# Kernel optimization log

Hardware: AMD Instinct MI355X
Metric: run time of the kernel (lower is better)

## Reference

```python
import jax, jax.numpy as jnp
import numpy as np

B, N, F, E = 4, 256, 128, 128
HID = 128      # link ConvLSTM hidden channels
L_PROP = 2     # propagate_layers
SUB, AFF = 10, 12


def setup_inputs() -> dict:
    key = jax.random.key(0)
    ks = jax.random.split(key, 16)
    s = 0.02
    inp = dict(
        edge_features=jax.random.normal(ks[0], (B, E, N, N), jnp.float32),
        node_features=jax.random.normal(ks[1], (B, F, N), jnp.float32),
        adj_mat=jax.random.uniform(ks[2], (B, N, N), dtype=jnp.float32),
        node_labels=jnp.zeros((B, N, AFF), jnp.float32),
        args=0,
    )
    # GraphConvLSTM link function: two 1x1-conv LSTM cells + 1x1 output conv
    inp['W_lstm0'] = s * jax.random.normal(ks[3], (4 * HID, E + HID), jnp.float32)
    inp['b_lstm0'] = jnp.zeros((4 * HID,), jnp.float32)
    inp['W_lstm1'] = s * jax.random.normal(ks[4], (4 * HID, HID + HID), jnp.float32)
    inp['b_lstm1'] = jnp.zeros((4 * HID,), jnp.float32)
    inp['W_link_out'] = s * jax.random.normal(ks[5], (1, HID), jnp.float32)
    inp['b_link_out'] = jnp.zeros((1,), jnp.float32)
    # linear_concat message: Linear(2F+E -> E)
    inp['W_msg'] = s * jax.random.normal(ks[6], (E, 2 * F + E), jnp.float32)
    inp['b_msg'] = jnp.zeros((E,), jnp.float32)
    # two GRU update functions (node 0 vs other nodes), input E, hidden F
    inp['Wih0'] = s * jax.random.normal(ks[7], (3 * F, E), jnp.float32)
    inp['Whh0'] = s * jax.random.normal(ks[8], (3 * F, F), jnp.float32)
    inp['bih0'] = jnp.zeros((3 * F,), jnp.float32)
    inp['bhh0'] = jnp.zeros((3 * F,), jnp.float32)
    inp['Wih1'] = s * jax.random.normal(ks[9], (3 * F, E), jnp.float32)
    inp['Whh1'] = s * jax.random.normal(ks[10], (3 * F, F), jnp.float32)
    inp['bih1'] = jnp.zeros((3 * F,), jnp.float32)
    inp['bhh1'] = jnp.zeros((3 * F,), jnp.float32)
    # fc_soft_max readouts
    inp['Wr0'] = s * jax.random.normal(ks[11], (SUB, F), jnp.float32)
    inp['br0'] = jnp.zeros((SUB,), jnp.float32)
    inp['Wr1'] = s * jax.random.normal(ks[12], (AFF, F), jnp.float32)
    inp['br1'] = jnp.zeros((AFF,), jnp.float32)
    return inp


def _link_fun(he, Ws, bs, Wo, bo):
    # he: [B, C, N, N] edge states -> predicted soft adjacency [B, N, N]
    x = he
    for W, b in zip(Ws, bs):
        hid = W.shape[0] // 4
        h0 = jnp.zeros(x.shape[:1] + (hid,) + x.shape[2:], x.dtype)
        xc = jnp.concatenate([x, h0], axis=1)
        g = jnp.einsum('oc,bcvw->bovw', W, xc) + b[None, :, None, None]
        i_g, f_g, g_g, o_g = jnp.split(g, 4, axis=1)
        c = jax.nn.sigmoid(i_g) * jnp.tanh(g_g)  # forget*c0 vanishes (c0=0)
        x = jax.nn.sigmoid(o_g) * jnp.tanh(c)
    a = jnp.einsum('oc,bcvw->bovw', Wo, x) + bo[None, :, None, None]
    return jax.nn.sigmoid(a)[:, 0]  # [B, N, N]


def _messages(node_features, edge_features, A, W_msg, b_msg):
    # X[b,:,w,i] = concat(h_i, h_w, e[i,w]); m[b,o,w,i] = (W_msg X + b) * A[b,i,w]
    hv = jnp.broadcast_to(node_features[:, :, None, :], (B, F, N, N))
    hw = jnp.broadcast_to(node_features[:, :, :, None], (B, F, N, N))
    ev = jnp.swapaxes(edge_features, 2, 3)
    X = jnp.concatenate([hv, hw, ev], axis=1)  # [B, 2F+E, N, N]
    m = jnp.einsum('of,bfwi->bowi', W_msg, X) + b_msg[None, :, None, None]
    return m * jnp.swapaxes(A, 1, 2)[:, None, :, :]


def _gru(x, h, Wih, Whh, bih, bhh):
    gi = x @ Wih.T + bih
    gh = h @ Whh.T + bhh
    ir, iz, inn = jnp.split(gi, 3, axis=-1)
    hr, hz, hn = jnp.split(gh, 3, axis=-1)
    r = jax.nn.sigmoid(ir + hr)
    z = jax.nn.sigmoid(iz + hz)
    n = jnp.tanh(inn + r * hn)
    return (1.0 - z) * n + z * h


def reference(edge_features, node_features, adj_mat, node_labels, args,
              W_lstm0, b_lstm0, W_lstm1, b_lstm1, W_link_out, b_link_out,
              W_msg, b_msg, Wih0, Whh0, bih0, bhh0, Wih1, Whh1, bih1, bhh1,
              Wr0, br0, Wr1, br1):
    he = edge_features  # hidden_edge_states[0]
    A = None
    m_sum = None
    for _ in range(L_PROP):
        A = _link_fun(he, [W_lstm0, W_lstm1], [b_lstm0, b_lstm1], W_link_out, b_link_out)
        m = _messages(node_features, edge_features, A, W_msg, b_msg)
        he = m                     # hidden_edge_states[r+1][:,:,:,i] = m_v
        m_sum = m.sum(axis=2)      # [B, E, N]: sum over source nodes w
    # GRU update (hidden node states are never rewritten in the source, so
    # only the last round's update feeds the readout)
    h = jnp.swapaxes(node_features, 1, 2)  # [B, N, F]
    x = jnp.swapaxes(m_sum, 1, 2)          # [B, N, E]
    h_new0 = _gru(x[:, :1], h[:, :1], Wih0, Whh0, bih0, bhh0)  # node 0
    h_new1 = _gru(x[:, 1:], h[:, 1:], Wih1, Whh1, bih1, bhh1)  # other nodes
    out0 = jax.nn.log_softmax(h_new0[:, 0] @ Wr0.T + br0, axis=-1)  # [B, SUB]
    out1 = jax.nn.log_softmax(h_new1 @ Wr1.T + br1, axis=-1)        # [B, N-1, AFF]
    pred = jnp.zeros(node_labels.shape, node_labels.dtype)
    pred = pred.at[:, 0, :SUB].set(out0)
    pred = pred.at[:, 1:, :].set(out1)
    return A, pred
```

## Files before the change

### kernel.cpp

```cpp
#include <hip/hip_runtime.h>

#define CH 128
#define PIXTOT (4*256*256)
#define L2E 1.4426950408889634f

typedef unsigned short u16;
typedef short short8 __attribute__((ext_vector_type(8)));
typedef float f32x4 __attribute__((ext_vector_type(4)));

__device__ __forceinline__ float bf2f(u16 u){ return __uint_as_float(((unsigned)u)<<16); }
__device__ __forceinline__ u16 f2bf(float f){
  return (u16)((__float_as_uint(f) + 0x8000u) >> 16);
}
__device__ __forceinline__ unsigned pk2(float a, float b){
  return (unsigned)f2bf(a) | ((unsigned)f2bf(b) << 16);
}
__device__ __forceinline__ float fexp2(float x){ return __builtin_amdgcn_exp2f(x); }
__device__ __forceinline__ float frcp(float x){ return __builtin_amdgcn_rcpf(x); }
__device__ __forceinline__ float sigm(float x){ return frcp(1.f + fexp2(-L2E*x)); }
__device__ __forceinline__ float tanh_f(float x){ return 1.f - 2.f*frcp(fexp2(2.f*L2E*x)+1.f); }
__device__ __forceinline__ float pade_tanh(float c){
  float c2 = c*c, c4 = c2*c2;
  float p  = __builtin_fmaf(c2, 105.f, 945.f) + c4;
  float q  = __builtin_fmaf(c4, 15.f, __builtin_fmaf(c2, 420.f, 945.f));
  return c * p * frcp(q);
}

__global__ __launch_bounds__(256) void wcvt_kernel(
    const float* __restrict__ W0, const float* __restrict__ bl0,
    const float* __restrict__ W1, const float* __restrict__ bl1,
    const float* __restrict__ Wm,
    const float* __restrict__ Wih1, const float* __restrict__ Whh1,
    u16* __restrict__ W0c, u16* __restrict__ W1c,
    float* __restrict__ b0c, float* __restrict__ b1c,
    u16* __restrict__ Wmc, float* __restrict__ W3T,
    u16* __restrict__ Wuv, u16* __restrict__ Wg1)
{
  int idx = blockIdx.x*256 + threadIdx.x;
  int col = idx & 127;
  if (idx < 49152){
    int row = idx >> 7;
    int slot = row >> 7;
    int src = (row < 128) ? row : row + 128;
    float s = (slot == 1) ? (2.f*L2E) : (-L2E);
    W0c[idx] = f2bf(W0[(size_t)src*256 + col] * s);
    W1c[idx] = f2bf(W1[(size_t)src*256 + col] * s);
  }
  if (idx < 16384){
    int o = idx >> 7, k = col;
    float w = Wm[(size_t)o*384 + 256 + k];
    Wmc[idx] = f2bf(w);
    W3T[(size_t)k*128 + o] = w;
  }
  if (idx < 32768){
    int row = idx >> 7;
    Wuv[idx] = (row < 128) ? f2bf(Wm[(size_t)row*384 + col])
                           : f2bf(Wm[(size_t)(row-128)*384 + 128 + col]);
  }
  {
    int row = idx >> 7;
    Wg1[idx] = (row < 384) ? f2bf(Wih1[(size_t)row*128 + col])
                           : f2bf(Whh1[(size_t)(row-384)*128 + col]);
  }
  if (idx < 384){
    int row = idx;
    int src = (row < 128) ? row : row + 128;
    float s = ((row>>7) == 1) ? (2.f*L2E) : (-L2E);
    b0c[idx] = bl0[src] * s;
    b1c[idx] = bl1[src] * s;
  }
}

__device__ __forceinline__ void stage_cmaj(
    const float* __restrict__ base, u16 (*xs)[136], int t)
{
  const int cg = t >> 4, pg = t & 15;
  const int c0 = cg*8, p0 = pg*4;
  float v[8][4];
  #pragma unroll
  for (int cc=0; cc<8; cc++){
    const f32x4 f = *(const f32x4*)(base + (size_t)(c0+cc)*256 + p0);
    v[cc][0]=f[0]; v[cc][1]=f[1]; v[cc][2]=f[2]; v[cc][3]=f[3];
  }
  #pragma unroll
  for (int pp=0; pp<4; pp++){
    unsigned d[4];
    #pragma unroll
    for (int q=0; q<4; q++) d[q] = pk2(v[2*q][pp], v[2*q+1][pp]);
    *(uint4*)&xs[p0+pp][c0] = *(const uint4*)d;
  }
}

__global__ __launch_bounds__(256) void uvmfma_kernel(
    const float* __restrict__ nf, const u16* __restrict__ Wuv,
    const float* __restrict__ bmsg, float* __restrict__ U, float* __restrict__ V)
{
  const int b = blockIdx.x >> 2, i0 = (blockIdx.x & 3) * 64;
  __shared__ u16 xs[64][136];
  const int t = threadIdx.x;
  stage_cmaj(nf + (size_t)b*CH*256 + i0, xs, t);
  __syncthreads();
  const int wv = t >> 6, lane = t & 63, lm = lane & 15, quad = lane >> 4;
  f32x4 acc[4][4];
  #pragma unroll
  for (int rs=0; rs<4; rs++)
    #pragma unroll
    for (int nt=0; nt<4; nt++){ f32x4 z={0.f,0.f,0.f,0.f}; acc[rs][nt]=z; }
  #pragma unroll
  for (int k0=0; k0<128; k0+=32){
    short8 bfr[4];
    #pragma unroll
    for (int nt=0; nt<4; nt++)
      bfr[nt] = *(const short8*)&xs[nt*16+lm][k0 + quad*8];
    #pragma unroll
    for (int rs=0; rs<4; rs++){
      const short8 afr = *(const short8*)(Wuv + ((size_t)(wv*64 + rs*16 + lm))*128 + k0 + quad*8);
      #pragma unroll
      for (int nt=0; nt<4; nt++)
        acc[rs][nt] = __builtin_amdgcn_mfma_f32_16x16x32_bf16(afr, bfr[nt], acc[rs][nt], 0,0,0);
    }
  }
  #pragma unroll
  for (int rs=0; rs<4; rs++){
    const int row0 = wv*64 + rs*16 + quad*4;
    #pragma unroll
    for (int nt=0; nt<4; nt++){
      const int i = i0 + nt*16 + lm;
      f32x4 o = acc[rs][nt];
      if (row0 < 128){
        const f32x4 bm = *(const f32x4*)(bmsg + row0);
        o[0]+=bm[0]; o[1]+=bm[1]; o[2]+=bm[2]; o[3]+=bm[3];
        *(f32x4*)(U + ((size_t)(b*256 + i))*CH + row0) = o;
      } else {
        *(f32x4*)(V + ((size_t)(b*256 + i))*CH + row0 - 128) = o;
      }
    }
  }
}

template<bool LAST>
__device__ __forceinline__ void lstm_layer(
    const u16 (*xin)[136], u16 (*xout)[136],
    const u16* __restrict__ W, const float* __restrict__ Bc,
    int oc0, int lm, int quad, const float woc[2][4], float* partial)
{
  float tp[2][4][4];
  #pragma unroll
  for (int g=0; g<3; g++){
    f32x4 acc[2][4];
    #pragma unroll
    for (int rs=0; rs<2; rs++)
      #pragma unroll
      for (int nt=0; nt<4; nt++){ f32x4 z={0.f,0.f,0.f,0.f}; acc[rs][nt]=z; }
    #pragma unroll
    for (int k0=0; k0<128; k0+=32){
      short8 bfr[4];
      #pragma unroll
      for (int nt=0; nt<4; nt++)
        bfr[nt] = *(const short8*)&xin[nt*16+lm][k0 + quad*8];
      #pragma unroll
      for (int rs=0; rs<2; rs++){
        const short8 afr = *(const short8*)(W + ((size_t)(g*128 + oc0 + rs*16 + lm))*128 + k0 + quad*8);
        #pragma unroll
        for (int nt=0; nt<4; nt++)
          acc[rs][nt] = __builtin_amdgcn_mfma_f32_16x16x32_bf16(afr, bfr[nt], acc[rs][nt], 0,0,0);
      }
    }
    #pragma unroll
    for (int rs=0; rs<2; rs++){
      float bi[4];
      #pragma unroll
      for (int r=0; r<4; r++) bi[r] = Bc[g*128 + oc0 + rs*16 + quad*4 + r];
      #pragma unroll
      for (int nt=0; nt<4; nt++){
        if (g == 0){
          #pragma unroll
          for (int r=0; r<4; r++)
            tp[rs][nt][r] = frcp(1.f + fexp2(acc[rs][nt][r] + bi[r]));
        } else if (g == 1){
          #pragma unroll
          for (int r=0; r<4; r++){
            float e = fexp2(fminf(acc[rs][nt][r] + bi[r], 80.f));
            float c = tp[rs][nt][r] * (e - 1.f) * frcp(e + 1.f);
            tp[rs][nt][r] = pade_tanh(c);
          }
        } else {
          float xo[4];
          #pragma unroll
          for (int r=0; r<4; r++)
            xo[r] = tp[rs][nt][r] * frcp(1.f + fexp2(acc[rs][nt][r] + bi[r]));
          if (LAST){
            #pragma unroll
            for (int r=0; r<4; r++)
              partial[nt] = __builtin_fmaf(xo[r], woc[rs][r], partial[nt]);
          } else {
            ushort4 w4;
            #pragma unroll
            for (int r=0; r<4; r++) ((u16*)&w4)[r] = f2bf(xo[r]);
            *(ushort4*)&xout[nt*16+lm][oc0 + rs*16 + quad*4] = w4;
          }
        }
      }
    }
  }
}

template<int MODE>
__global__ __launch_bounds__(256, 3) void link_kernel(
    const float* __restrict__ edge, const float* __restrict__ A1,
    const float* __restrict__ U, const float* __restrict__ V,
    const u16* __restrict__ Wmc,
    const u16* __restrict__ W0c, const float* __restrict__ B0c,
    const u16* __restrict__ W1c, const float* __restrict__ B1c,
    const float* __restrict__ Wo, const float* __restrict__ Bo,
    float* __restrict__ Aout, float* __restrict__ outA, float* __restrict__ A2nat)
{
  __shared__ u16 xs[64][136];
  __shared__ u16 ys[64][136];
  __shared__ float red[64][17];
  const int t = threadIdx.x;
  const int Q0 = blockIdx.x * 64;
  const int b = Q0 >> 16, q1 = (Q0 >> 8) & 255, w0 = Q0 & 255;
  stage_cmaj(edge + ((size_t)b*CH*256 + q1)*256 + w0, xs, t);
  const int wv = t >> 6, lane = t & 63, lm = lane & 15, quad = lane >> 4;
  const int oc0 = wv*32;
  float woc[2][4];
  #pragma unroll
  for (int rs=0; rs<2; rs++){
    const f32x4 wv4 = *(const f32x4*)(Wo + oc0 + rs*16 + quad*4);
    #pragma unroll
    for (int r=0; r<4; r++) woc[rs][r] = wv4[r];
  }
  __syncthreads();
  if (MODE){
    f32x4 acc[2][4];
    #pragma unroll
    for (int rs=0; rs<2; rs++)
      #pragma unroll
      for (int nt=0; nt<4; nt++){ f32x4 z={0.f,0.f,0.f,0.f}; acc[rs][nt]=z; }
    #pragma unroll
    for (int k0=0; k0<128; k0+=32){
      short8 bfr[4];
      #pragma unroll
      for (int nt=0; nt<4; nt++)
        bfr[nt] = *(const short8*)&xs[nt*16+lm][k0 + quad*8];
      #pragma unroll
      for (int rs=0; rs<2; rs++){
        const short8 afr = *(const short8*)(Wmc + ((size_t)(oc0 + rs*16 + lm))*128 + k0 + quad*8);
        #pragma unroll
        for (int nt=0; nt<4; nt++)
          acc[rs][nt] = __builtin_amdgcn_mfma_f32_16x16x32_bf16(afr, bfr[nt], acc[rs][nt], 0,0,0);
      }
    }
    #pragma unroll
    for (int rs=0; rs<2; rs++){
      const int o0 = oc0 + rs*16 + quad*4;
      const f32x4 ug = *(const f32x4*)(U + ((size_t)(b*256 + q1))*CH + o0);
      #pragma unroll
      for (int nt=0; nt<4; nt++){
        const int px = nt*16 + lm;
        const float a1 = A1[Q0 + px];
        const f32x4 vg = *(const f32x4*)(V + ((size_t)(b*256 + w0 + px))*CH + o0);
        ushort4 w4;
        #pragma unroll
        for (int r=0; r<4; r++)
          ((u16*)&w4)[r] = f2bf((acc[rs][nt][r] + ug[r] + vg[r]) * a1);
        *(ushort4*)&ys[px][o0] = w4;
      }
    }
    __syncthreads();
  }
  const u16 (*in0)[136] = MODE ? (const u16(*)[136])ys : (const u16(*)[136])xs;
  u16 (*buf)[136] = MODE ? xs : ys;
  float partial[4] = {0.f, 0.f, 0.f, 0.f};
  lstm_layer<false>(in0, buf, W0c, B0c, oc0, lm, quad, woc, partial);
  __syncthreads();
  lstm_layer<true>((const u16(*)[136])buf, (u16(*)[136])nullptr, W1c, B1c, oc0, lm, quad, woc, partial);
  #pragma unroll
  for (int nt=0; nt<4; nt++) red[nt*16+lm][wv*4+quad] = partial[nt];
  __syncthreads();
  if (t < 64){
    float s = Bo[0];
    #pragma unroll
    for (int k=0; k<16; k++) s += red[t][k];
    const float sg = sigm(s);
    Aout[Q0 + t] = sg;
    if (MODE){
      const size_t p = (size_t)b*65536 + (size_t)(w0 + t)*256 + q1;
      outA[p]  = sg;
      A2nat[p] = sg;
    }
  }
}

__global__ __launch_bounds__(256) void se_kernel(
    const float* __restrict__ edge, const float* __restrict__ A2nat,
    float* __restrict__ s_e, float* __restrict__ sA)
{
  const int b = blockIdx.x >> 8, i = blockIdx.x & 255;
  __shared__ float al[256];
  __shared__ float sb[128][9];
  __shared__ float rr[64];
  const int t = threadIdx.x;
  al[t] = A2nat[((size_t)(b*256 + i))*256 + t];
  __syncthreads();
  const int seg = t & 7, cb = t >> 3;
  #pragma unroll
  for (int cc=0; cc<4; cc++){
    const int c = cc*32 + cb;
    const float* src = edge + (((size_t)(b*CH + c))*256 + i)*256;
    float s = 0.f;
    #pragma unroll
    for (int j=0; j<8; j++){
      const int idx = j*32 + seg*4;
      const f32x4 v = *(const f32x4*)(src + idx);
      s += v[0]*al[idx] + v[1]*al[idx+1] + v[2]*al[idx+2] + v[3]*al[idx+3];
    }
    sb[c][seg] = s;
  }
  if (t < 64) rr[t] = al[t] + al[t+64] + al[t+128] + al[t+192];
  __syncthreads();
  if (t < 128){
    float s = 0.f;
    #pragma unroll
    for (int k=0; k<8; k++) s += sb[t][k];
    s_e[((size_t)(b*256 + i))*CH + t] = s;
  }
  if (t == 0){
    float sa = 0.f;
    for (int k=0; k<64; k++) sa += rr[k];
    sA[b*256 + i] = sa;
  }
}

__global__ __launch_bounds__(128) void mfinal_kernel(
    const float* __restrict__ s_e, const float* __restrict__ sA,
    const float* __restrict__ A2nat, const float* __restrict__ V,
    const float* __restrict__ W3T, const float* __restrict__ U,
    float* __restrict__ msum)
{
  const int b = blockIdx.x >> 8, i = blockIdx.x & 255;
  __shared__ float se_s[128];
  __shared__ float al[256];
  const int t = threadIdx.x;
  se_s[t] = s_e[((size_t)(b*256 + i))*CH + t];
  al[t]       = A2nat[((size_t)(b*256 + i))*256 + t];
  al[t + 128] = A2nat[((size_t)(b*256 + i))*256 + t + 128];
  __syncthreads();
  float s = U[((size_t)(b*256 + i))*CH + t] * sA[b*256 + i];
  const float* w3 = W3T + t;
  #pragma unroll 8
  for (int k=0; k<128; k++)
    s += w3[(size_t)k*128] * se_s[k];
  const float* vp = V + ((size_t)(b*256))*CH + t;
  #pragma unroll 8
  for (int w=0; w<256; w++)
    s += al[w] * vp[(size_t)w*CH];
  msum[((size_t)(b*256 + i))*CH + t] = s;
}

__global__ __launch_bounds__(256) void gg_kernel(
    const float* __restrict__ msum, const float* __restrict__ nf,
    const u16* __restrict__ Wg1, float* __restrict__ G)
{
  const int b = blockIdx.x >> 2, n0 = (blockIdx.x & 3) * 64;
  __shared__ u16 xs[64][136];
  __shared__ u16 hs[64][136];
  const int t = threadIdx.x;
  {
    const int p = t >> 2, seg = (t & 3) * 32;
    const float* src = msum + ((size_t)(b*256 + n0 + p))*CH + seg;
    #pragma unroll
    for (int jj=0; jj<2; jj++){
      unsigned d[8];
      #pragma unroll
      for (int q=0; q<4; q++){
        const f32x4 v = *(const f32x4*)(src + jj*16 + q*4);
        d[q*2]   = pk2(v[0], v[1]);
        d[q*2+1] = pk2(v[2], v[3]);
      }
      *(uint4*)&xs[p][seg + jj*16]     = *(const uint4*)d;
      *(uint4*)&xs[p][seg + jj*16 + 8] = *(const uint4*)(d+4);
    }
  }
  stage_cmaj(nf + (size_t)b*CH*256 + n0, hs, t);
  __syncthreads();
  const int wv = t >> 6, lane = t & 63, lm = lane & 15, quad = lane >> 4;
  #pragma unroll
  for (int half=0; half<2; half++){
    const u16 (*in)[136] = half ? (const u16(*)[136])hs : (const u16(*)[136])xs;
    const u16* Wb = Wg1 + (size_t)half*384*128;
    #pragma unroll
    for (int rs=0; rs<6; rs++){
      f32x4 acc[4];
      #pragma unroll
      for (int nt=0; nt<4; nt++){ f32x4 z={0.f,0.f,0.f,0.f}; acc[nt]=z; }
      #pragma unroll
      for (int k0=0; k0<128; k0+=32){
        short8 bfr[4];
        #pragma unroll
        for (int nt=0; nt<4; nt++)
          bfr[nt] = *(const short8*)&in[nt*16+lm][k0 + quad*8];
        const short8 afr = *(const short8*)(Wb + ((size_t)(wv*96 + rs*16 + lm))*128 + k0 + quad*8);
        #pragma unroll
        for (int nt=0; nt<4; nt++)
          acc[nt] = __builtin_amdgcn_mfma_f32_16x16x32_bf16(afr, bfr[nt], acc[nt], 0,0,0);
      }
      #pragma unroll
      for (int nt=0; nt<4; nt++){
        const int n = n0 + nt*16 + lm;
        *(f32x4*)(G + ((size_t)(b*256 + n))*768 + half*384 + wv*96 + rs*16 + quad*4) = acc[nt];
      }
    }
  }
}

__global__ __launch_bounds__(128) void k5b_kernel(
    const float* __restrict__ G, const float* __restrict__ msum,
    const float* __restrict__ nf,
    const float* __restrict__ Wih0, const float* __restrict__ Whh0,
    const float* __restrict__ bih0, const float* __restrict__ bhh0,
    const float* __restrict__ bih1, const float* __restrict__ bhh1,
    const float* __restrict__ Wr0, const float* __restrict__ br0,
    const float* __restrict__ Wr1, const float* __restrict__ br1,
    float* __restrict__ outp)
{
  const int blk = blockIdx.x, b = blk >> 8, n = blk & 255;
  __shared__ float gl[768];
  __shared__ float xsh[128], hsh[128], hnew[128], lg[16];
  const int t = threadIdx.x;
  hsh[t] = nf[((size_t)(b*CH + t))*256 + n];
  float gi[3], gh[3];
  if (n == 0){
    xsh[t] = msum[((size_t)(b*256 + n))*CH + t];
    __syncthreads();
    #pragma unroll
    for (int prt=0; prt<3; prt++){
      int row = prt*128 + t;
      const float* wi_ = Wih0 + (size_t)row*CH;
      const float* wh_ = Whh0 + (size_t)row*CH;
      float si = 0.f, sh2 = 0.f;
      for (int k=0; k<128; k+=4){
        f32x4 wv1 = *(const f32x4*)(wi_ + k);
        f32x4 wv2 = *(const f32x4*)(wh_ + k);
        #pragma unroll
        for (int j=0; j<4; j++){ si += wv1[j]*xsh[k+j]; sh2 += wv2[j]*hsh[k+j]; }
      }
      gi[prt] = si + bih0[row];
      gh[prt] = sh2 + bhh0[row];
    }
  } else {
    #pragma unroll
    for (int p=0; p<6; p++) gl[p*128 + t] = G[((size_t)(b*256 + n))*768 + p*128 + t];
    __syncthreads();
    #pragma unroll
    for (int prt=0; prt<3; prt++){
      gi[prt] = gl[prt*128 + t] + bih1[prt*128 + t];
      gh[prt] = gl[384 + prt*128 + t] + bhh1[prt*128 + t];
    }
  }
  float r  = sigm(gi[0] + gh[0]);
  float z  = sigm(gi[1] + gh[1]);
  float ng = tanh_f(gi[2] + r*gh[2]);
  hnew[t] = (1.f - z)*ng + z*hsh[t];
  __syncthreads();
  const int K = n ? 12 : 10;
  const float* Wr = n ? Wr1 : Wr0;  const float* br = n ? br1 : br0;
  if (t < K){
    const float* wr_ = Wr + (size_t)t*CH;
    float s = 0.f;
    for (int k=0; k<128; k+=4){
      f32x4 wv1 = *(const f32x4*)(wr_ + k);
      #pragma unroll
      for (int j=0; j<4; j++) s += wv1[j]*hnew[k+j];
    }
    lg[t] = s + br[t];
  }
  __syncthreads();
  if (t < 12){
    float o = 0.f;
    if (t < K){
      float mx = -1e30f;
      for (int j=0; j<K; j++) mx = fmaxf(mx, lg[j]);
      float se = 0.f;
      for (int j=0; j<K; j++) se += __expf(lg[j] - mx);
      o = lg[t] - mx - __logf(se);
    }
    outp[((size_t)(b*256 + n))*12 + t] = o;
  }
}

extern "C" void kernel_launch(void* const* d_in, const int* in_sizes, int n_in,
                              void* d_out, int out_size, void* d_ws, size_t ws_size,
                              hipStream_t stream)
{
  (void)in_sizes; (void)n_in; (void)out_size; (void)ws_size;
  const float* edge = (const float*)d_in[0];
  const float* nf   = (const float*)d_in[1];
  const float* Wl0  = (const float*)d_in[5];
  const float* bl0  = (const float*)d_in[6];
  const float* Wl1  = (const float*)d_in[7];
  const float* bl1  = (const float*)d_in[8];
  const float* Wlo  = (const float*)d_in[9];
  const float* blo  = (const float*)d_in[10];
  const float* Wmsg = (const float*)d_in[11];
  const float* bmsg = (const float*)d_in[12];
  const float* Wih0 = (const float*)d_in[13];
  const float* Whh0 = (const float*)d_in[14];
  const float* bih0 = (const float*)d_in[15];
  const float* bhh0 = (const float*)d_in[16];
  const float* Wih1 = (const float*)d_in[17];
  const float* Whh1 = (const float*)d_in[18];
  const float* bih1 = (const float*)d_in[19];
  const float* bhh1 = (const float*)d_in[20];
  const float* Wr0  = (const float*)d_in[21];
  const float* br0  = (const float*)d_in[22];
  const float* Wr1  = (const float*)d_in[23];
  const float* br1  = (const float*)d_in[24];

  char* ws = (char*)d_ws;
  float* A1v   = (float*)(ws);
  float* A2nat = (float*)(ws + 1048576);
  float* U     = (float*)(ws + 2097152);
  float* V     = (float*)(ws + 2621440);
  float* msum  = (float*)(ws + 3145728);
  float* s_e   = (float*)(ws + 3670016);
  float* sAr   = (float*)(ws + 4194304);
  u16*   W0c   = (u16*)(ws + 4198400);
  u16*   W1c   = (u16*)(ws + 4296704);
  u16*   Wmc   = (u16*)(ws + 4395008);
  float* b0c   = (float*)(ws + 4427776);
  float* b1c   = (float*)(ws + 4429312);
  u16*   Wuv   = (u16*)(ws + 4430848);
  u16*   Wg1   = (u16*)(ws + 4496384);
  float* W3T   = (float*)(ws + 4692992);
  float* G     = (float*)(ws);

  float* outA = (float*)d_out;
  float* outP = outA + (size_t)PIXTOT;

  wcvt_kernel<<<dim3(384), dim3(256), 0, stream>>>(
      Wl0, bl0, Wl1, bl1, Wmsg, Wih1, Whh1,
      W0c, W1c, b0c, b1c, Wmc, W3T, Wuv, Wg1);
  uvmfma_kernel<<<dim3(16), dim3(256), 0, stream>>>(nf, Wuv, bmsg, U, V);
  link_kernel<0><<<dim3(PIXTOT/64), dim3(256), 0, stream>>>(
      edge, (const float*)nullptr, U, V, Wmc, W0c, b0c, W1c, b1c, Wlo, blo,
      A1v, (float*)nullptr, (float*)nullptr);
  link_kernel<1><<<dim3(PIXTOT/64), dim3(256), 0, stream>>>(
      edge, A1v, U, V, Wmc, W0c, b0c, W1c, b1c, Wlo, blo,
      A1v, outA, A2nat);
  se_kernel<<<dim3(4*256), dim3(256), 0, stream>>>(edge, A2nat, s_e, sAr);
  mfinal_kernel<<<dim3(4*256), dim3(128), 0, stream>>>(
      s_e, sAr, A2nat, V, W3T, U, msum);
  gg_kernel<<<dim3(16), dim3(256), 0, stream>>>(msum, nf, Wg1, G);
  k5b_kernel<<<dim3(4*256), dim3(128), 0, stream>>>(
      G, msum, nf, Wih0, Whh0, bih0, bhh0, bih1, bhh1,
      Wr0, br0, Wr1, br1, outP);
}
```

Measured before the change: 619.6 us.

## Fold message linear into LSTM layer-0 weights for second link pass

For the second link pass, the message projection is folded algebraically into the first LSTM layer. W0·Wm is precomputed, and per-node U/V tables are projected through W0, so the message GEMM and its staging are replaced by table lookups scaled by A1. The LSTM gate math is also reorganised to drop a reciprocal per gate. The new path depends on workspace size, adds two small precompute kernels, and reads fp32 tables with per-pixel strided loads. It also composes weights before bf16 rounding, which changes numerics slightly.

```diff
diff --git a/kernel.cpp b/kernel.cpp
--- a/kernel.cpp
+++ b/kernel.cpp
@@ -19,12 +19,6 @@
 __device__ __forceinline__ float frcp(float x){ return __builtin_amdgcn_rcpf(x); }
 __device__ __forceinline__ float sigm(float x){ return frcp(1.f + fexp2(-L2E*x)); }
 __device__ __forceinline__ float tanh_f(float x){ return 1.f - 2.f*frcp(fexp2(2.f*L2E*x)+1.f); }
-__device__ __forceinline__ float pade_tanh(float c){
-  float c2 = c*c, c4 = c2*c2;
-  float p  = __builtin_fmaf(c2, 105.f, 945.f) + c4;
-  float q  = __builtin_fmaf(c4, 15.f, __builtin_fmaf(c2, 420.f, 945.f));
-  return c * p * frcp(q);
-}
 
 __global__ __launch_bounds__(256) void wcvt_kernel(
     const float* __restrict__ W0, const float* __restrict__ bl0,
@@ -71,6 +65,22 @@
   }
 }
 
+__global__ __launch_bounds__(256) void wcomp_kernel(
+    const float* __restrict__ W0, const float* __restrict__ Wm,
+    u16* __restrict__ W0m)
+{
+  int idx = blockIdx.x*256 + threadIdx.x;
+  int row = idx >> 7, k = idx & 127;
+  int src = (row < 128) ? row : row + 128;
+  float s = ((row>>7) == 1) ? (2.f*L2E) : (-L2E);
+  const float* wr = W0 + (size_t)src*256;
+  const float* wc = Wm + 256 + k;
+  float acc = 0.f;
+  #pragma unroll 8
+  for (int o=0; o<128; o++) acc += wr[o] * wc[(size_t)o*384];
+  W0m[idx] = f2bf(acc * s);
+}
+
 __device__ __forceinline__ void stage_cmaj(
     const float* __restrict__ base, u16 (*xs)[136], int t)
 {
@@ -88,6 +98,24 @@
     #pragma unroll
     for (int q=0; q<4; q++) d[q] = pk2(v[2*q][pp], v[2*q+1][pp]);
     *(uint4*)&xs[p0+pp][c0] = *(const uint4*)d;
+  }
+}
+__device__ __forceinline__ void stage_rmaj(
+    const float* __restrict__ base, u16 (*xs)[136], int t)
+{
+  const int p = t >> 2, seg = (t & 3) * 32;
+  const float* src = base + (size_t)p*CH + seg;
+  #pragma unroll
+  for (int jj=0; jj<2; jj++){
+    unsigned d[8];
+    #pragma unroll
+    for (int q=0; q<4; q++){
+      const f32x4 v = *(const f32x4*)(src + jj*16 + q*4);
+      d[q*2]   = pk2(v[0], v[1]);
+      d[q*2+1] = pk2(v[2], v[3]);
+    }
+    *(uint4*)&xs[p][seg + jj*16]     = *(const uint4*)d;
+    *(uint4*)&xs[p][seg + jj*16 + 8] = *(const uint4*)(d+4);
   }
 }
 
@@ -138,11 +166,50 @@
   }
 }
 
-template<bool LAST>
+__global__ __launch_bounds__(256) void wtab_kernel(
+    const float* __restrict__ U, const float* __restrict__ V,
+    const u16* __restrict__ W0c, float* __restrict__ tabU, float* __restrict__ tabV)
+{
+  const int blk = blockIdx.x;
+  const int which = blk >> 4, b = (blk >> 2) & 3, n0 = (blk & 3)*64;
+  const float* T = which ? V : U;
+  float* Out = which ? tabV : tabU;
+  __shared__ u16 xs[64][136];
+  const int t = threadIdx.x;
+  stage_rmaj(T + ((size_t)(b*256 + n0))*CH, xs, t);
+  __syncthreads();
+  const int wv = t >> 6, lane = t & 63, lm = lane & 15, quad = lane >> 4;
+  #pragma unroll
+  for (int rs=0; rs<6; rs++){
+    f32x4 acc[4];
+    #pragma unroll
+    for (int nt=0; nt<4; nt++){ f32x4 z={0.f,0.f,0.f,0.f}; acc[nt]=z; }
+    #pragma unroll
+    for (int k0=0; k0<128; k0+=32){
+      short8 bfr[4];
+      #pragma unroll
+      for (int nt=0; nt<4; nt++)
+        bfr[nt] = *(const short8*)&xs[nt*16+lm][k0 + quad*8];
+      const short8 afr = *(const short8*)(W0c + ((size_t)(wv*96 + rs*16 + lm))*128 + k0 + quad*8);
+      #pragma unroll
+      for (int nt=0; nt<4; nt++)
+        acc[nt] = __builtin_amdgcn_mfma_f32_16x16x32_bf16(afr, bfr[nt], acc[nt], 0,0,0);
+    }
+    #pragma unroll
+    for (int nt=0; nt<4; nt++){
+      const int n = n0 + nt*16 + lm;
+      *(f32x4*)(Out + ((size_t)(b*256 + n))*384 + wv*96 + rs*16 + quad*4) = acc[nt];
+    }
+  }
+}
+
+template<int PRE, bool LAST>
 __device__ __forceinline__ void lstm_layer(
     const u16 (*xin)[136], u16 (*xout)[136],
     const u16* __restrict__ W, const float* __restrict__ Bc,
-    int oc0, int lm, int quad, const float woc[2][4], float* partial)
+    int oc0, int lm, int quad, const float woc[2][4], float* partial,
+    const float* __restrict__ tu, const float* __restrict__ tvb,
+    const float* __restrict__ a1s)
 {
   float tp[2][4][4];
   #pragma unroll
@@ -168,27 +235,46 @@
     }
     #pragma unroll
     for (int rs=0; rs<2; rs++){
+      const int ro = g*128 + oc0 + rs*16 + quad*4;
       float bi[4];
       #pragma unroll
-      for (int r=0; r<4; r++) bi[r] = Bc[g*128 + oc0 + rs*16 + quad*4 + r];
+      for (int r=0; r<4; r++) bi[r] = Bc[ro + r];
+      f32x4 tug;
+      if (PRE) tug = *(const f32x4*)(tu + ro);
       #pragma unroll
       for (int nt=0; nt<4; nt++){
+        const int px = nt*16 + lm;
+        float pre[4];
+        if (PRE){
+          const f32x4 tv = *(const f32x4*)(tvb + (size_t)px*384 + ro);
+          const float a1 = a1s[px];
+          #pragma unroll
+          for (int r=0; r<4; r++)
+            pre[r] = __builtin_fmaf(a1, acc[rs][nt][r] + tug[r] + tv[r], bi[r]);
+        } else {
+          #pragma unroll
+          for (int r=0; r<4; r++) pre[r] = acc[rs][nt][r] + bi[r];
+        }
         if (g == 0){
           #pragma unroll
-          for (int r=0; r<4; r++)
-            tp[rs][nt][r] = frcp(1.f + fexp2(acc[rs][nt][r] + bi[r]));
+          for (int r=0; r<4; r++) tp[rs][nt][r] = fexp2(pre[r]);
         } else if (g == 1){
           #pragma unroll
           for (int r=0; r<4; r++){
-            float e = fexp2(fminf(acc[rs][nt][r] + bi[r], 80.f));
-            float c = tp[rs][nt][r] * (e - 1.f) * frcp(e + 1.f);
-            tp[rs][nt][r] = pade_tanh(c);
+            float bb = fexp2(fminf(pre[r], 80.f));
+            tp[rs][nt][r] = (bb - 1.f) * frcp((1.f + tp[rs][nt][r]) * (bb + 1.f));
           }
         } else {
           float xo[4];
           #pragma unroll
-          for (int r=0; r<4; r++)
-            xo[r] = tp[rs][nt][r] * frcp(1.f + fexp2(acc[rs][nt][r] + bi[r]));
+          for (int r=0; r<4; r++){
+            float f  = fexp2(pre[r]);
+            float c  = tp[rs][nt][r];
+            float c2 = c*c, c4 = c2*c2;
+            float p  = __builtin_fmaf(c2, 105.f, 945.f) + c4;
+            float q  = __builtin_fmaf(c4, 15.f, __builtin_fmaf(c2, 420.f, 945.f));
+            xo[r] = c * p * frcp(q * (1.f + f));
+          }
           if (LAST){
             #pragma unroll
             for (int r=0; r<4; r++)
@@ -197,7 +283,7 @@
             ushort4 w4;
             #pragma unroll
             for (int r=0; r<4; r++) ((u16*)&w4)[r] = f2bf(xo[r]);
-            *(ushort4*)&xout[nt*16+lm][oc0 + rs*16 + quad*4] = w4;
+            *(ushort4*)&xout[px][oc0 + rs*16 + quad*4] = w4;
           }
         }
       }
@@ -213,15 +299,18 @@
     const u16* __restrict__ W0c, const float* __restrict__ B0c,
     const u16* __restrict__ W1c, const float* __restrict__ B1c,
     const float* __restrict__ Wo, const float* __restrict__ Bo,
+    const float* __restrict__ tabU, const float* __restrict__ tabV,
     float* __restrict__ Aout, float* __restrict__ outA, float* __restrict__ A2nat)
 {
   __shared__ u16 xs[64][136];
   __shared__ u16 ys[64][136];
   __shared__ float red[64][17];
+  float* a1s = (float*)red;
   const int t = threadIdx.x;
   const int Q0 = blockIdx.x * 64;
   const int b = Q0 >> 16, q1 = (Q0 >> 8) & 255, w0 = Q0 & 255;
   stage_cmaj(edge + ((size_t)b*CH*256 + q1)*256 + w0, xs, t);
+  if (MODE == 2 && t < 64) a1s[t] = A1[Q0 + t];
   const int wv = t >> 6, lane = t & 63, lm = lane & 15, quad = lane >> 4;
   const int oc0 = wv*32;
   float woc[2][4];
@@ -232,7 +321,7 @@
     for (int r=0; r<4; r++) woc[rs][r] = wv4[r];
   }
   __syncthreads();
-  if (MODE){
+  if (MODE == 1){
     f32x4 acc[2][4];
     #pragma unroll
     for (int rs=0; rs<2; rs++)
@@ -270,12 +359,27 @@
     }
     __syncthreads();
   }
-  const u16 (*in0)[136] = MODE ? (const u16(*)[136])ys : (const u16(*)[136])xs;
-  u16 (*buf)[136] = MODE ? xs : ys;
   float partial[4] = {0.f, 0.f, 0.f, 0.f};
-  lstm_layer<false>(in0, buf, W0c, B0c, oc0, lm, quad, woc, partial);
-  __syncthreads();
-  lstm_layer<true>((const u16(*)[136])buf, (u16(*)[136])nullptr, W1c, B1c, oc0, lm, quad, woc, partial);
+  if (MODE == 1){
+    lstm_layer<0,false>((const u16(*)[136])ys, xs, W0c, B0c, oc0, lm, quad, woc, partial,
+                        nullptr, nullptr, nullptr);
+    __syncthreads();
+    lstm_layer<0,true>((const u16(*)[136])xs, nullptr, W1c, B1c, oc0, lm, quad, woc, partial,
+                       nullptr, nullptr, nullptr);
+  } else if (MODE == 2){
+    lstm_layer<1,false>((const u16(*)[136])xs, ys, W0c , B0c, oc0, lm, quad, woc, partial,
+                        tabU + ((size_t)(b*256 + q1))*384,
+                        tabV + ((size_t)(b*256 + w0))*384, a1s);
+    __syncthreads();
+    lstm_layer<0,true>((const u16(*)[136])ys, nullptr, W1c, B1c, oc0, lm, quad, woc, partial,
+                       nullptr, nullptr, nullptr);
+  } else {
+    lstm_layer<0,false>((const u16(*)[136])xs, ys, W0c, B0c, oc0, lm, quad, woc, partial,
+                        nullptr, nullptr, nullptr);
+    __syncthreads();
+    lstm_layer<0,true>((const u16(*)[136])ys, nullptr, W1c, B1c, oc0, lm, quad, woc, partial,
+                       nullptr, nullptr, nullptr);
+  }
   #pragma unroll
   for (int nt=0; nt<4; nt++) red[nt*16+lm][wv*4+quad] = partial[nt];
   __syncthreads();
@@ -285,7 +389,7 @@
     for (int k=0; k<16; k++) s += red[t][k];
     const float sg = sigm(s);
     Aout[Q0 + t] = sg;
-    if (MODE){
+    if (MODE != 0){
       const size_t p = (size_t)b*65536 + (size_t)(w0 + t)*256 + q1;
       outA[p]  = sg;
       A2nat[p] = sg;
@@ -367,22 +471,7 @@
   __shared__ u16 xs[64][136];
   __shared__ u16 hs[64][136];
   const int t = threadIdx.x;
-  {
-    const int p = t >> 2, seg = (t & 3) * 32;
-    const float* src = msum + ((size_t)(b*256 + n0 + p))*CH + seg;
-    #pragma unroll
-    for (int jj=0; jj<2; jj++){
-      unsigned d[8];
-      #pragma unroll
-      for (int q=0; q<4; q++){
-        const f32x4 v = *(const f32x4*)(src + jj*16 + q*4);
-        d[q*2]   = pk2(v[0], v[1]);
-        d[q*2+1] = pk2(v[2], v[3]);
-      }
-      *(uint4*)&xs[p][seg + jj*16]     = *(const uint4*)d;
-      *(uint4*)&xs[p][seg + jj*16 + 8] = *(const uint4*)(d+4);
-    }
-  }
+  stage_rmaj(msum + ((size_t)(b*256 + n0))*CH, xs, t);
   stage_cmaj(nf + (size_t)b*CH*256 + n0, hs, t);
   __syncthreads();
   const int wv = t >> 6, lane = t & 63, lm = lane & 15, quad = lane >> 4;
@@ -494,7 +583,7 @@
                               void* d_out, int out_size, void* d_ws, size_t ws_size,
                               hipStream_t stream)
 {
-  (void)in_sizes; (void)n_in; (void)out_size; (void)ws_size;
+  (void)in_sizes; (void)n_in; (void)out_size;
   const float* edge = (const float*)d_in[0];
   const float* nf   = (const float*)d_in[1];
   const float* Wl0  = (const float*)d_in[5];
@@ -534,7 +623,12 @@
   u16*   Wuv   = (u16*)(ws + 4430848);
   u16*   Wg1   = (u16*)(ws + 4496384);
   float* W3T   = (float*)(ws + 4692992);
+  u16*   W0m   = (u16*)(ws + 4758528);
+  float* tabU  = (float*)(ws + 4856832);
+  float* tabV  = (float*)(ws + 6429696);
   float* G     = (float*)(ws);
+
+  const bool big = ws_size >= 8100000;
 
   float* outA = (float*)d_out;
   float* outP = outA + (size_t)PIXTOT;
@@ -543,12 +637,23 @@
       Wl0, bl0, Wl1, bl1, Wmsg, Wih1, Whh1,
       W0c, W1c, b0c, b1c, Wmc, W3T, Wuv, Wg1);
   uvmfma_kernel<<<dim3(16), dim3(256), 0, stream>>>(nf, Wuv, bmsg, U, V);
+  if (big){
+    wcomp_kernel<<<dim3(192), dim3(256), 0, stream>>>(Wl0, Wmsg, W0m);
+    wtab_kernel<<<dim3(32), dim3(256), 0, stream>>>(U, V, W0c, tabU, tabV);
+  }
   link_kernel<0><<<dim3(PIXTOT/64), dim3(256), 0, stream>>>(
       edge, (const float*)nullptr, U, V, Wmc, W0c, b0c, W1c, b1c, Wlo, blo,
+      (const float*)nullptr, (const float*)nullptr,
       A1v, (float*)nullptr, (float*)nullptr);
-  link_kernel<1><<<dim3(PIXTOT/64), dim3(256), 0, stream>>>(
-      edge, A1v, U, V, Wmc, W0c, b0c, W1c, b1c, Wlo, blo,
-      A1v, outA, A2nat);
+  if (big){
+    link_kernel<2><<<dim3(PIXTOT/64), dim3(256), 0, stream>>>(
+        edge, A1v, U, V, Wmc, W0m, b0c, W1c, b1c, Wlo, blo,
+        tabU, tabV, A1v, outA, A2nat);
+  } else {
+    link_kernel<1><<<dim3(PIXTOT/64), dim3(256), 0, stream>>>(
+        edge, A1v, U, V, Wmc, W0c, b0c, W1c, b1c, Wlo, blo,
+        (const float*)nullptr, (const float*)nullptr, A1v, outA, A2nat);
+  }
   se_kernel<<<dim3(4*256), dim3(256), 0, stream>>>(edge, A2nat, s_e, sAr);
   mfinal_kernel<<<dim3(4*256), dim3(128), 0, stream>>>(
       s_e, sAr, A2nat, V, W3T, U, msum);
```

New measurement: 651.7 us. 1.05x slower.
